# Performance work log

Measured on AMD Instinct MI355X. Metric: run time of the kernel, lower is better.

## Reference

```python
import jax, jax.numpy as jnp
import numpy as np

D_MODEL, D_STATE, D_CONV, EXPAND = 1024, 16, 4, 2
D_INNER = EXPAND * D_MODEL            # 2048
DT_RANK = -(-D_MODEL // 16)           # ceil(d_model/16) = 64
B_SZ, L_SEQ = 2, 2048


def setup_inputs() -> dict:
    key = jax.random.key(0)
    ks = jax.random.split(key, 8)
    s = 0.02
    x = jax.random.normal(ks[0], (B_SZ, L_SEQ, D_MODEL), dtype=jnp.float32)
    W_in = jax.random.normal(ks[1], (D_MODEL, 2 * D_INNER), dtype=jnp.float32) * s
    conv_w = jax.random.normal(ks[2], (D_INNER, 1, D_CONV), dtype=jnp.float32) * 0.1  # depthwise (O,I/g,K)
    conv_b = jnp.zeros((D_INNER,), dtype=jnp.float32)
    W_x = jax.random.normal(ks[3], (D_INNER, DT_RANK + 2 * D_STATE), dtype=jnp.float32) * s
    W_dt = jax.random.normal(ks[4], (DT_RANK, D_INNER), dtype=jnp.float32) * s
    b_dt = jax.random.normal(ks[5], (D_INNER,), dtype=jnp.float32) * 0.1
    A_log = jnp.log(jnp.tile(jnp.arange(1, D_STATE + 1, dtype=jnp.float32), (D_INNER, 1)))  # (d_in, n)
    D_param = jnp.ones((D_INNER,), dtype=jnp.float32)
    W_out = jax.random.normal(ks[6], (D_INNER, D_MODEL), dtype=jnp.float32) * s
    return {"x": x, "W_in": W_in, "conv_w": conv_w, "conv_b": conv_b,
            "W_x": W_x, "W_dt": W_dt, "b_dt": b_dt, "A_log": A_log,
            "D_param": D_param, "W_out": W_out}


def _mamba(x, W_in, conv_w, conv_b, W_x, W_dt, b_dt, A_log, D_param, W_out):
    b, l, _ = x.shape
    d_in, n = A_log.shape
    dt_rank = W_dt.shape[0]
    d_conv = conv_w.shape[-1]

    xr = x @ W_in                                  # (b, l, 2*d_in)
    xs, res = xr[..., :d_in], xr[..., d_in:]

    # causal depthwise conv1d (left pad d_conv-1, truncate to l)
    xc = jnp.transpose(xs, (0, 2, 1))              # (b, d_in, l)
    xc = jax.lax.conv_general_dilated(
        xc, conv_w, window_strides=(1,), padding=[(d_conv - 1, 0)],
        dimension_numbers=("NCH", "OIH", "NCH"), feature_group_count=d_in)
    xc = xc + conv_b[None, :, None]
    xc = jnp.transpose(xc, (0, 2, 1))              # (b, l, d_in)
    xc = jax.nn.silu(xc)

    # SSM parameterization
    x_dbl = xc @ W_x                               # (b, l, dt_rank + 2n)
    delta = jax.nn.softplus(x_dbl[..., :dt_rank] @ W_dt + b_dt)   # (b, l, d_in)
    Bm = x_dbl[..., dt_rank:dt_rank + n]           # (b, l, n)
    Cm = x_dbl[..., dt_rank + n:]                  # (b, l, n)
    A = -jnp.exp(A_log)                            # (d_in, n)

    deltaA = jnp.exp(jnp.einsum("bld,dn->bldn", delta, A))        # (b, l, d_in, n)
    dBu = jnp.einsum("bld,bld,bln->bldn", delta, xc, Bm)          # (b, l, d_in, n)

    def step(h, inp):
        dA_t, dBu_t, C_t = inp                     # (b,d,n), (b,d,n), (b,n)
        h = dA_t * h + dBu_t
        y_t = jnp.einsum("bdn,bn->bd", h, C_t)
        return h, y_t

    h0 = jnp.zeros((b, d_in, n), dtype=xc.dtype)
    _, ys = jax.lax.scan(
        step, h0,
        (jnp.transpose(deltaA, (1, 0, 2, 3)),
         jnp.transpose(dBu, (1, 0, 2, 3)),
         jnp.transpose(Cm, (1, 0, 2))))
    y = jnp.transpose(ys, (1, 0, 2)) + xc * D_param  # (b, l, d_in)

    y = y * jax.nn.silu(res)
    return y @ W_out                               # (b, l, d_model)


def reference(x, W_in, conv_w, conv_b, W_x, W_dt, b_dt, A_log, D_param, W_out):
    return _mamba(x, W_in, conv_w, conv_b, W_x, W_dt, b_dt, A_log, D_param, W_out)
```

## Files before the change

### kernel.cpp

```cpp
#include <hip/hip_runtime.h>
#include <math.h>

#define B_SZ    2
#define L_SEQ   2048
#define D_MODEL 1024
#define D_INNER 2048
#define D_STATE 16
#define DT_RANK 64
#define MM      (B_SZ * L_SEQ)
#define NCH     64
#define CLEN    (L_SEQ / NCH)
#define PFD     8

typedef _Float16 h8v __attribute__((ext_vector_type(8)));
typedef _Float16 h4v __attribute__((ext_vector_type(4)));
typedef float f32x4 __attribute__((ext_vector_type(4)));

__device__ __forceinline__ void gload16(const void* g, void* l) {
    __builtin_amdgcn_global_load_lds((const __attribute__((address_space(1))) void*)g,
                                     (__attribute__((address_space(3))) void*)l, 16, 0, 0);
}

__global__ __launch_bounds__(256) void prep(const float* __restrict__ x,
                                            _Float16* __restrict__ xf16,
                                            const float* __restrict__ W_in,
                                            _Float16* __restrict__ WinT,
                                            const float* __restrict__ W_x,
                                            _Float16* __restrict__ WxT,
                                            const float* __restrict__ W_dt,
                                            _Float16* __restrict__ WdtT,
                                            const float* __restrict__ W_out,
                                            _Float16* __restrict__ WoutT,
                                            const float* __restrict__ cw,
                                            float* __restrict__ cwT) {
    __shared__ float t[32][33];
    const int b = blockIdx.x;
    const float* W; _Float16* T; int K, N, tile;
    if (b < 4096)      { W = W_in;  T = WinT;  K = 1024; N = 4096; tile = b; }
    else if (b < 4288) { W = W_x;   T = WxT;   K = 2048; N = 96;   tile = b - 4096; }
    else if (b < 4416) { W = W_dt;  T = WdtT;  K = 64;   N = 2048; tile = b - 4288; }
    else if (b < 6464) { W = W_out; T = WoutT; K = 2048; N = 1024; tile = b - 4416; }
    else if (b < 10560) {
        int idx = (b - 6464) * 256 + threadIdx.x;
        float4 v = ((const float4*)x)[idx];
        h4v h = {(_Float16)v.x, (_Float16)v.y, (_Float16)v.z, (_Float16)v.w};
        *(h4v*)(xf16 + (size_t)idx * 4) = h;
        return;
    } else {
        for (int i = threadIdx.x; i < D_INNER * 4; i += 256) {
            int d = i >> 2, k = i & 3;
            cwT[k * D_INNER + d] = cw[i];
        }
        return;
    }
    const int ntx = N / 32;
    const int k0 = (tile / ntx) * 32, n0 = (tile % ntx) * 32;
    #pragma unroll
    for (int i = 0; i < 4; ++i) {
        int idx = threadIdx.x + i * 256;
        int r = idx >> 5, c = idx & 31;
        t[r][c] = W[(size_t)(k0 + r) * N + n0 + c];
    }
    __syncthreads();
    #pragma unroll
    for (int i = 0; i < 4; ++i) {
        int idx = threadIdx.x + i * 256;
        int n = idx >> 5, k = idx & 31;
        T[(size_t)(n0 + n) * K + k0 + k] = (_Float16)t[k][n];
    }
}

#define LDA_(mi, ks) (*(const h8v*)(smb + cb_ + rowA + (mi) * 2048 + ((ks) ? ps1 : ps0)))
#define LDB_(ni, ks) (*(const h8v*)(smb + cb_ + 32768 + rowB + (ni) * 2048 + ((ks) ? ps1 : ps0)))
#define PH(m0, m1) \
    _Pragma("unroll") \
    for (int ni = 0; ni < 4; ++ni) { \
        acc[m0][ni] = __builtin_amdgcn_mfma_f32_16x16x32_f16(aF0, bF[2 * ni],     acc[m0][ni], 0, 0, 0); \
        acc[m0][ni] = __builtin_amdgcn_mfma_f32_16x16x32_f16(aF1, bF[2 * ni + 1], acc[m0][ni], 0, 0, 0); \
        acc[m1][ni] = __builtin_amdgcn_mfma_f32_16x16x32_f16(aF2, bF[2 * ni],     acc[m1][ni], 0, 0, 0); \
        acc[m1][ni] = __builtin_amdgcn_mfma_f32_16x16x32_f16(aF3, bF[2 * ni + 1], acc[m1][ni], 0, 0, 0); \
    }

__global__ __launch_bounds__(512, 2) void gemm_k1(const _Float16* __restrict__ A,
                                                  const _Float16* __restrict__ Bt,
                                                  _Float16* __restrict__ H,
                                                  _Float16* __restrict__ Hg) {
    __shared__ _Float16 smem[65536];
    char* smb = (char*)smem;

    const int tid  = threadIdx.x;
    const int wave = tid >> 6, lane = tid & 63;
    const int wm = wave >> 2, wn = wave & 3;
    const int lm = lane & 15, lq = lane >> 4;
    const int bm = blockIdx.y * 256, bn = blockIdx.x * 256;

    const int ps0 = ((lq)     ^ (lm & 7)) << 4;
    const int ps1 = ((lq + 4) ^ (lm & 7)) << 4;
    const int rowA = (wm * 128 + lm) << 7;
    const int rowB = (wn * 64 + lm) << 7;

    const int srow  = lane >> 3;
    const int sslot = (lane & 7) ^ srow;
    const _Float16* pA = A  + (size_t)(bm + wave * 32 + srow) * 1024 + sslot * 8;
    const _Float16* pB = Bt + (size_t)(bn + wave * 32 + srow) * 1024 + sslot * 8;
    char* dA = smb + wave * 4096;
    char* dB = smb + 32768 + wave * 4096;

    f32x4 acc[8][4];
    #pragma unroll
    for (int i = 0; i < 8; ++i)
        #pragma unroll
        for (int j = 0; j < 4; ++j) acc[i][j] = (f32x4){0.f, 0.f, 0.f, 0.f};

    #pragma unroll
    for (int q = 0; q < 4; ++q) {
        gload16(pA + q * 8192, dA + q * 1024);
        gload16(pB + q * 8192, dB + q * 1024);
    }
    asm volatile("s_waitcnt vmcnt(0)" ::: "memory");
    __builtin_amdgcn_s_barrier();

    int cb_ = 0;
    for (int t = 0; t < 16; ++t) {
        const int nb_ = 65536 - cb_;
        const bool pf = (t < 15);
        const size_t kn = (size_t)(t + 1) * 64;

        h8v aF0, aF1, aF2, aF3;
        h8v bF[8];

        aF0 = LDA_(0, 0); aF1 = LDA_(0, 1); aF2 = LDA_(1, 0); aF3 = LDA_(1, 1);
        #pragma unroll
        for (int ni = 0; ni < 4; ++ni) { bF[2 * ni] = LDB_(ni, 0); bF[2 * ni + 1] = LDB_(ni, 1); }
        if (pf) {
            #pragma unroll
            for (int q = 0; q < 4; ++q) gload16(pA + kn + q * 8192, dA + nb_ + q * 1024);
        }
        __builtin_amdgcn_s_barrier();
        asm volatile("s_waitcnt lgkmcnt(0)" ::: "memory");
        __builtin_amdgcn_s_setprio(1);
        PH(0, 1);
        __builtin_amdgcn_s_setprio(0);
        __builtin_amdgcn_s_barrier();

        aF0 = LDA_(2, 0); aF1 = LDA_(2, 1); aF2 = LDA_(3, 0); aF3 = LDA_(3, 1);
        if (pf) {
            #pragma unroll
            for (int q = 0; q < 4; ++q) gload16(pB + kn + q * 8192, dB + nb_ + q * 1024);
        }
        __builtin_amdgcn_s_barrier();
        asm volatile("s_waitcnt lgkmcnt(0)" ::: "memory");
        __builtin_amdgcn_s_setprio(1);
        PH(2, 3);
        __builtin_amdgcn_s_setprio(0);
        __builtin_amdgcn_s_barrier();

        aF0 = LDA_(4, 0); aF1 = LDA_(4, 1); aF2 = LDA_(5, 0); aF3 = LDA_(5, 1);
        __builtin_amdgcn_s_barrier();
        asm volatile("s_waitcnt lgkmcnt(0)" ::: "memory");
        __builtin_amdgcn_s_setprio(1);
        PH(4, 5);
        __builtin_amdgcn_s_setprio(0);
        __builtin_amdgcn_s_barrier();

        aF0 = LDA_(6, 0); aF1 = LDA_(6, 1); aF2 = LDA_(7, 0); aF3 = LDA_(7, 1);
        asm volatile("s_waitcnt vmcnt(4)" ::: "memory");
        __builtin_amdgcn_s_barrier();
        asm volatile("s_waitcnt lgkmcnt(0)" ::: "memory");
        __builtin_amdgcn_s_setprio(1);
        PH(6, 7);
        __builtin_amdgcn_s_setprio(0);
        asm volatile("s_waitcnt vmcnt(0)" ::: "memory");
        __builtin_amdgcn_s_barrier();

        cb_ = nb_;
    }

    _Float16* ep = smem + wave * 2048;
    const bool gate = (bn >= 2048);
    _Float16* dst = gate ? Hg : H;
    const int cbase = bn + wn * 64 - (gate ? 2048 : 0);
    #pragma unroll
    for (int mi = 0; mi < 8; ++mi) {
        #pragma unroll
        for (int ni = 0; ni < 4; ++ni)
            #pragma unroll
            for (int r = 0; r < 4; ++r) {
                float v = acc[mi][ni][r];
                if (gate) v = v / (1.f + __expf(-v));
                ep[(lq * 4 + r) * 72 + ni * 16 + lm] = (_Float16)v;
            }
        int rowb = bm + wm * 128 + mi * 16;
        #pragma unroll
        for (int i = 0; i < 2; ++i) {
            int ch = lane + 64 * i;
            int row = ch >> 3, c8 = (ch & 7) * 8;
            *(h8v*)&dst[(size_t)(rowb + row) * 2048 + cbase + c8] =
                *(const h8v*)&ep[row * 72 + c8];
        }
    }
}
#undef LDA_
#undef LDB_
#undef PH

template<int EPI>
__global__ __launch_bounds__(256) void gemm_f16(const _Float16* __restrict__ A,
                                                const _Float16* __restrict__ Bt,
                                                const float* __restrict__ bias,
                                                float* __restrict__ C,
                                                _Float16* __restrict__ H,
                                                _Float16* __restrict__ Hg,
                                                int M, int N, int K, int ldc) {
    __shared__ _Float16 smemh[16384];

    const int tid = threadIdx.x;
    const int wave = tid >> 6, lane = tid & 63;
    const int bm = blockIdx.y * 128, bn = blockIdx.x * 128;

    const int lrow = lane >> 2, pc = lane & 3;
    const int ar = wave * 32 + lrow;
    const size_t gA = (size_t)(bm + ar) * K + ((pc ^ ((ar >> 1) & 3)) * 8);
    const size_t gB = (size_t)(bn + ar) * K + ((pc ^ ((ar >> 1) & 3)) * 8);
    const int lofs = (wave * 32) * 32;

    const int lm = lane & 15, lq = lane >> 4;
    const int rofs = (lq ^ ((lm >> 1) & 3)) * 8;
    const int wm = (wave >> 1) * 64, wn = (wave & 1) * 64;

    f32x4 acc[4][4];
    #pragma unroll
    for (int i = 0; i < 4; ++i)
        #pragma unroll
        for (int j = 0; j < 4; ++j) acc[i][j] = (f32x4){0.f, 0.f, 0.f, 0.f};

    gload16(A + gA, smemh + lofs);
    gload16(A + gA + (size_t)16 * K, smemh + lofs + 16 * 32);
    gload16(Bt + gB, smemh + 8192 + lofs);
    gload16(Bt + gB + (size_t)16 * K, smemh + 8192 + lofs + 16 * 32);
    __syncthreads();

    int kb = 0;
    for (int k0 = 0; k0 < K; k0 += 32, kb ^= 1) {
        if (k0 + 32 < K) {
            int nb = kb ^ 1;
            gload16(A + gA + k0 + 32, smemh + nb * 4096 + lofs);
            gload16(A + gA + k0 + 32 + (size_t)16 * K, smemh + nb * 4096 + lofs + 16 * 32);
            gload16(Bt + gB + k0 + 32, smemh + 8192 + nb * 4096 + lofs);
            gload16(Bt + gB + k0 + 32 + (size_t)16 * K, smemh + 8192 + nb * 4096 + lofs + 16 * 32);
        }

        const _Float16* sA = smemh + kb * 4096;
        const _Float16* sB = smemh + 8192 + kb * 4096;
        h8v fa[4], fb[4];
        #pragma unroll
        for (int i = 0; i < 4; ++i) {
            fa[i] = *(const h8v*)&sA[(wm + i * 16 + lm) * 32 + rofs];
            fb[i] = *(const h8v*)&sB[(wn + i * 16 + lm) * 32 + rofs];
        }
        #pragma unroll
        for (int mi = 0; mi < 4; ++mi)
            #pragma unroll
            for (int ni = 0; ni < 4; ++ni)
                acc[mi][ni] = __builtin_amdgcn_mfma_f32_16x16x32_f16(fa[mi], fb[ni], acc[mi][ni], 0, 0, 0);
        __syncthreads();
    }

    if (EPI == 0) {
        float* ep = (float*)smemh + wave * 1088;
        #pragma unroll
        for (int mi = 0; mi < 4; ++mi) {
            #pragma unroll
            for (int ni = 0; ni < 4; ++ni)
                #pragma unroll
                for (int r = 0; r < 4; ++r)
                    ep[(lq * 4 + r) * 68 + ni * 16 + lm] = acc[mi][ni][r];
            int rowb = bm + wm + mi * 16;
            #pragma unroll
            for (int i = 0; i < 4; ++i) {
                int ch = lane + 64 * i;
                int row = ch >> 4, c4 = (ch & 15) * 4;
                *(float4*)&C[(size_t)(rowb + row) * ldc + bn + wn + c4] =
                    *(const float4*)&ep[row * 68 + c4];
            }
        }
    } else {
        _Float16* ep = smemh + wave * 1152;
        const bool gate = (EPI == 2) && (bn >= 2048);
        _Float16* dst = gate ? Hg : H;
        const int cb = bn + wn - (gate ? 2048 : 0);
        #pragma unroll
        for (int mi = 0; mi < 4; ++mi) {
            #pragma unroll
            for (int ni = 0; ni < 4; ++ni) {
                int col = bn + wn + ni * 16 + lm;
                #pragma unroll
                for (int r = 0; r < 4; ++r) {
                    float v = acc[mi][ni][r];
                    if (EPI == 1) {
                        float a = v + bias[col];
                        v = (a > 20.f) ? a : log1pf(__expf(a));
                    } else if (gate) {
                        v = v / (1.f + __expf(-v));
                    }
                    ep[(lq * 4 + r) * 72 + ni * 16 + lm] = (_Float16)v;
                }
            }
            int rowb = bm + wm + mi * 16;
            #pragma unroll
            for (int i = 0; i < 2; ++i) {
                int ch = lane + 64 * i;
                int row = ch >> 3, c8 = (ch & 7) * 8;
                *(h8v*)&dst[(size_t)(rowb + row) * ldc + cb + c8] =
                    *(const h8v*)&ep[row * 72 + c8];
            }
        }
    }
}

__global__ __launch_bounds__(256) void gemm_xd(const _Float16* __restrict__ xch,
                                               const _Float16* __restrict__ WxT,
                                               _Float16* __restrict__ xdh,
                                               float* __restrict__ Bm,
                                               float* __restrict__ Cm) {
    __shared__ _Float16 sA[64 * 32];
    __shared__ _Float16 sB[96 * 32];
    const int tid = threadIdx.x;
    const int m0 = blockIdx.x * 64;
    const int wave = tid >> 6, lane = tid & 63;
    const int lm = lane & 15, lq = lane >> 4;
    const int rofs = (lq ^ ((lm >> 1) & 3)) * 8;

    const int wr = tid >> 2, wc = tid & 3, c0 = wc * 8;
    const int wofsA = wr * 32 + ((wc ^ ((wr >> 1) & 3)) * 8);
    const int wr2 = 64 + wr;
    const int wofsB2 = wr2 * 32 + ((wc ^ ((wr2 >> 1) & 3)) * 8);

    f32x4 acc[6];
    #pragma unroll
    for (int i = 0; i < 6; ++i) acc[i] = (f32x4){0.f, 0.f, 0.f, 0.f};

    h8v pA = *(const h8v*)(xch + (size_t)(m0 + wr) * D_INNER + c0);
    h8v pB0 = *(const h8v*)(WxT + (size_t)wr * D_INNER + c0);
    h8v pB1 = (tid < 128) ? *(const h8v*)(WxT + (size_t)wr2 * D_INNER + c0) : (h8v)0;

    for (int k0 = 0; k0 < D_INNER; k0 += 32) {
        *(h8v*)&sA[wofsA] = pA;
        *(h8v*)&sB[wofsA] = pB0;
        if (tid < 128) *(h8v*)&sB[wofsB2] = pB1;
        __syncthreads();

        if (k0 + 32 < D_INNER) {
            int kk = k0 + 32 + c0;
            pA = *(const h8v*)(xch + (size_t)(m0 + wr) * D_INNER + kk);
            pB0 = *(const h8v*)(WxT + (size_t)wr * D_INNER + kk);
            if (tid < 128) pB1 = *(const h8v*)(WxT + (size_t)wr2 * D_INNER + kk);
        }

        h8v fa = *(const h8v*)&sA[(wave * 16 + lm) * 32 + rofs];
        #pragma unroll
        for (int nf = 0; nf < 6; ++nf) {
            h8v fb = *(const h8v*)&sB[(nf * 16 + lm) * 32 + rofs];
            acc[nf] = __builtin_amdgcn_mfma_f32_16x16x32_f16(fa, fb, acc[nf], 0, 0, 0);
        }
        __syncthreads();
    }

    #pragma unroll
    for (int nf = 0; nf < 6; ++nf) {
        int col = nf * 16 + lm;
        #pragma unroll
        for (int r = 0; r < 4; ++r) {
            int row = m0 + wave * 16 + lq * 4 + r;
            float v = acc[nf][r];
            if (col < 64)      xdh[(size_t)row * 64 + col] = (_Float16)v;
            else if (col < 80) Bm[(size_t)row * 16 + (col - 64)] = v;
            else               Cm[(size_t)row * 16 + (col - 80)] = v;
        }
    }
}

__global__ __launch_bounds__(256) void conv_silu(const _Float16* __restrict__ xsh,
                                                 const float* __restrict__ cwT,
                                                 const float* __restrict__ cb,
                                                 _Float16* __restrict__ xch) {
    int idx = blockIdx.x * 256 + threadIdx.x;
    int d0 = (idx * 8) & (D_INNER - 1);
    int m  = (idx * 8) >> 11;
    int l  = m & (L_SEQ - 1);
    float acc[8];
    {
        float4 c0 = *(const float4*)&cb[d0];
        float4 c1 = *(const float4*)&cb[d0 + 4];
        acc[0] = c0.x; acc[1] = c0.y; acc[2] = c0.z; acc[3] = c0.w;
        acc[4] = c1.x; acc[5] = c1.y; acc[6] = c1.z; acc[7] = c1.w;
    }
    #pragma unroll
    for (int k = 0; k < 4; ++k) {
        int ll = l - 3 + k;
        if (ll >= 0) {
            h8v v = *(const h8v*)(xsh + (size_t)(m - 3 + k) * D_INNER + d0);
            float4 w0 = *(const float4*)&cwT[k * D_INNER + d0];
            float4 w1 = *(const float4*)&cwT[k * D_INNER + d0 + 4];
            acc[0] += (float)v[0] * w0.x; acc[1] += (float)v[1] * w0.y;
            acc[2] += (float)v[2] * w0.z; acc[3] += (float)v[3] * w0.w;
            acc[4] += (float)v[4] * w1.x; acc[5] += (float)v[5] * w1.y;
            acc[6] += (float)v[6] * w1.z; acc[7] += (float)v[7] * w1.w;
        }
    }
    h8v o;
    #pragma unroll
    for (int j = 0; j < 8; ++j) {
        float s = acc[j] / (1.f + __expf(-acc[j]));
        o[j] = (_Float16)s;
    }
    *(h8v*)(xch + (size_t)idx * 8) = o;
}

__global__ __launch_bounds__(256) void scan_part1(const _Float16* __restrict__ deltah,
                                                  const _Float16* __restrict__ xch,
                                                  const float* __restrict__ Bm,
                                                  const float* __restrict__ A_log,
                                                  float* __restrict__ hlocal,
                                                  float* __restrict__ Ssum) {
    const int t = threadIdx.x;
    const int d = blockIdx.x * 256 + t;
    const int c = blockIdx.y;
    const int b = blockIdx.z;

    float An[16];
    {
        const float4* ap = (const float4*)(A_log + (size_t)d * 16);
        #pragma unroll
        for (int q = 0; q < 4; ++q) {
            float4 v = ap[q];
            An[q * 4 + 0] = -__expf(v.x); An[q * 4 + 1] = -__expf(v.y);
            An[q * 4 + 2] = -__expf(v.z); An[q * 4 + 3] = -__expf(v.w);
        }
    }
    const float An0 = An[0];
    bool fast = An0 < 0.f;
    #pragma unroll
    for (int n = 0; n < 16; ++n)
        fast = fast && (fabsf(An[n] - (float)(n + 1) * An0) < 1e-3f * fabsf(An[n]));

    __shared__ float sB[CLEN][16];
    {
        size_t l0 = (size_t)(b * L_SEQ + c * CLEN) * 16;
        #pragma unroll
        for (int i = 0; i < (CLEN * 16) / 256; ++i) {
            int idx = t + i * 256;
            sB[idx >> 4][idx & 15] = Bm[l0 + idx];
        }
    }
    __syncthreads();

    float h[16];
    #pragma unroll
    for (int n = 0; n < 16; ++n) h[n] = 0.f;
    float S = 0.f;

    size_t base = (size_t)(b * L_SEQ + c * CLEN) * D_INNER + d;
    float bd[PFD], bx[PFD];
    #pragma unroll
    for (int i = 0; i < PFD; ++i) {
        bd[i] = (float)deltah[base + (size_t)i * D_INNER];
        bx[i] = (float)xch[base + (size_t)i * D_INNER];
    }

    if (fast) {
        for (int jb = 0; jb < CLEN; jb += PFD) {
            #pragma unroll
            for (int i = 0; i < PFD; ++i) {
                int j = jb + i;
                float dv = bd[i], xv = bx[i];
                int jn = j + PFD;
                if (jn < CLEN) {
                    bd[i] = (float)deltah[base + (size_t)jn * D_INNER];
                    bx[i] = (float)xch[base + (size_t)jn * D_INNER];
                }
                S += dv;
                float dbx = dv * xv;
                float r = __expf(dv * An0);
                float pw = r;
                #pragma unroll
                for (int n = 0; n < 16; ++n) {
                    h[n] = pw * h[n] + dbx * sB[j][n];
                    pw *= r;
                }
            }
        }
    } else {
        for (int jb = 0; jb < CLEN; jb += PFD) {
            #pragma unroll
            for (int i = 0; i < PFD; ++i) {
                int j = jb + i;
                float dv = bd[i], xv = bx[i];
                int jn = j + PFD;
                if (jn < CLEN) {
                    bd[i] = (float)deltah[base + (size_t)jn * D_INNER];
                    bx[i] = (float)xch[base + (size_t)jn * D_INNER];
                }
                S += dv;
                float dbx = dv * xv;
                #pragma unroll
                for (int n = 0; n < 16; ++n)
                    h[n] = __expf(dv * An[n]) * h[n] + dbx * sB[j][n];
            }
        }
    }

    size_t o = ((size_t)(b * NCH + c) * D_INNER + d) * 16;
    float4* hp = (float4*)(hlocal + o);
    #pragma unroll
    for (int q = 0; q < 4; ++q)
        hp[q] = make_float4(h[q * 4], h[q * 4 + 1], h[q * 4 + 2], h[q * 4 + 3]);
    Ssum[(size_t)(b * NCH + c) * D_INNER + d] = S;
}

__global__ __launch_bounds__(256) void scan_combine(const float* __restrict__ hlocal,
                                                    const float* __restrict__ Ssum,
                                                    const float* __restrict__ A_log,
                                                    float* __restrict__ h0buf) {
    int gid = blockIdx.x * 256 + threadIdx.x;
    int n = gid & 15;
    int d = (gid >> 4) & (D_INNER - 1);
    int b = gid >> 15;
    float An = -__expf(A_log[(size_t)d * 16 + n]);
    float H = 0.f;
    float pS[4], pH[4];
    #pragma unroll
    for (int i = 0; i < 4; ++i) {
        size_t sc = (size_t)(b * NCH + i) * D_INNER + d;
        pS[i] = Ssum[sc];
        pH[i] = hlocal[sc * 16 + n];
    }
    for (int cb = 0; cb < NCH; cb += 4) {
        #pragma unroll
        for (int i = 0; i < 4; ++i) {
            int c = cb + i;
            float S = pS[i], hl = pH[i];
            int cn = c + 4;
            if (cn < NCH) {
                size_t sc = (size_t)(b * NCH + cn) * D_INNER + d;
                pS[i] = Ssum[sc];
                pH[i] = hlocal[sc * 16 + n];
            }
            size_t o = ((size_t)(b * NCH + c) * D_INNER + d) * 16 + n;
            h0buf[o] = H;
            H = __expf(An * S) * H + hl;
        }
    }
}

__global__ __launch_bounds__(256) void scan_part2(const _Float16* __restrict__ deltah,
                                                  const _Float16* __restrict__ xch,
                                                  const float* __restrict__ Bm,
                                                  const float* __restrict__ Cm,
                                                  const float* __restrict__ h0buf,
                                                  const float* __restrict__ A_log,
                                                  const float* __restrict__ Dp,
                                                  const _Float16* __restrict__ sresh,
                                                  _Float16* __restrict__ yhalf) {
    const int t = threadIdx.x;
    const int d = blockIdx.x * 256 + t;
    const int c = blockIdx.y;
    const int b = blockIdx.z;

    float An[16];
    {
        const float4* ap = (const float4*)(A_log + (size_t)d * 16);
        #pragma unroll
        for (int q = 0; q < 4; ++q) {
            float4 v = ap[q];
            An[q * 4 + 0] = -__expf(v.x); An[q * 4 + 1] = -__expf(v.y);
            An[q * 4 + 2] = -__expf(v.z); An[q * 4 + 3] = -__expf(v.w);
        }
    }
    const float An0 = An[0];
    bool fast = An0 < 0.f;
    #pragma unroll
    for (int n = 0; n < 16; ++n)
        fast = fast && (fabsf(An[n] - (float)(n + 1) * An0) < 1e-3f * fabsf(An[n]));

    __shared__ float sB[CLEN][16];
    __shared__ float sC[CLEN][16];
    {
        size_t l0 = (size_t)(b * L_SEQ + c * CLEN) * 16;
        #pragma unroll
        for (int i = 0; i < (CLEN * 16) / 256; ++i) {
            int idx = t + i * 256;
            sB[idx >> 4][idx & 15] = Bm[l0 + idx];
            sC[idx >> 4][idx & 15] = Cm[l0 + idx];
        }
    }
    __syncthreads();

    float h[16];
    {
        size_t o = ((size_t)(b * NCH + c) * D_INNER + d) * 16;
        const float4* hp = (const float4*)(h0buf + o);
        #pragma unroll
        for (int q = 0; q < 4; ++q) {
            float4 v = hp[q];
            h[q * 4 + 0] = v.x; h[q * 4 + 1] = v.y;
            h[q * 4 + 2] = v.z; h[q * 4 + 3] = v.w;
        }
    }
    const float Dv = Dp[d];

    size_t base = (size_t)(b * L_SEQ + c * CLEN) * D_INNER + d;
    float bd[PFD], bx[PFD], bg[PFD];
    #pragma unroll
    for (int i = 0; i < PFD; ++i) {
        bd[i] = (float)deltah[base + (size_t)i * D_INNER];
        bx[i] = (float)xch[base + (size_t)i * D_INNER];
        bg[i] = (float)sresh[base + (size_t)i * D_INNER];
    }

    if (fast) {
        for (int jb = 0; jb < CLEN; jb += PFD) {
            #pragma unroll
            for (int i = 0; i < PFD; ++i) {
                int j = jb + i;
                float dv = bd[i], xv = bx[i], gv = bg[i];
                int jn = j + PFD;
                if (jn < CLEN) {
                    bd[i] = (float)deltah[base + (size_t)jn * D_INNER];
                    bx[i] = (float)xch[base + (size_t)jn * D_INNER];
                    bg[i] = (float)sresh[base + (size_t)jn * D_INNER];
                }
                float dbx = dv * xv;
                float r = __expf(dv * An0);
                float pw = r;
                float y = 0.f;
                #pragma unroll
                for (int n = 0; n < 16; ++n) {
                    h[n] = pw * h[n] + dbx * sB[j][n];
                    y += h[n] * sC[j][n];
                    pw *= r;
                }
                float yv = (y + xv * Dv) * gv;
                yhalf[base + (size_t)j * D_INNER] = (_Float16)yv;
            }
        }
    } else {
        for (int jb = 0; jb < CLEN; jb += PFD) {
            #pragma unroll
            for (int i = 0; i < PFD; ++i) {
                int j = jb + i;
                float dv = bd[i], xv = bx[i], gv = bg[i];
                int jn = j + PFD;
                if (jn < CLEN) {
                    bd[i] = (float)deltah[base + (size_t)jn * D_INNER];
                    bx[i] = (float)xch[base + (size_t)jn * D_INNER];
                    bg[i] = (float)sresh[base + (size_t)jn * D_INNER];
                }
                float dbx = dv * xv;
                float y = 0.f;
                #pragma unroll
                for (int n = 0; n < 16; ++n) {
                    h[n] = __expf(dv * An[n]) * h[n] + dbx * sB[j][n];
                    y += h[n] * sC[j][n];
                }
                float yv = (y + xv * Dv) * gv;
                yhalf[base + (size_t)j * D_INNER] = (_Float16)yv;
            }
        }
    }
}

extern "C" void kernel_launch(void* const* d_in, const int* in_sizes, int n_in,
                              void* d_out, int out_size, void* d_ws, size_t ws_size,
                              hipStream_t stream) {
    const float* x      = (const float*)d_in[0];
    const float* W_in   = (const float*)d_in[1];
    const float* conv_w = (const float*)d_in[2];
    const float* conv_b = (const float*)d_in[3];
    const float* W_x    = (const float*)d_in[4];
    const float* W_dt   = (const float*)d_in[5];
    const float* b_dt   = (const float*)d_in[6];
    const float* A_log  = (const float*)d_in[7];
    const float* D_par  = (const float*)d_in[8];
    const float* W_out  = (const float*)d_in[9];
    float* out = (float*)d_out;

    char* wsb = (char*)d_ws;
    _Float16*  xsh    = (_Float16*)(wsb + 0);
    _Float16*  sresh  = (_Float16*)(wsb + 16777216);
    _Float16*  deltah = (_Float16*)(wsb + 33554432);
    _Float16*  xch    = (_Float16*)(wsb + 50331648);
    _Float16*  xf16   = (_Float16*)(wsb + 67108864);
    _Float16*  WinT   = (_Float16*)(wsb + 75497472);
    _Float16*  yhalf  = (_Float16*)(wsb + 67108864);
    _Float16*  WxT    = (_Float16*)(wsb + 83886080);
    _Float16*  WdtT   = (_Float16*)(wsb + 84279296);
    _Float16*  xdh    = (_Float16*)(wsb + 84541440);
    float*     Bbuf   = (float*)(wsb + 85065728);
    float*     Cbuf   = (float*)(wsb + 85327872);
    float*     Ssum   = (float*)(wsb + 85590016);
    float*     hloc   = (float*)(wsb + 86638592);
    float*     h0buf  = (float*)(wsb + 103415808);
    _Float16*  WoutT  = (_Float16*)(wsb + 120193024);
    float*     cwT    = (float*)(wsb + 124387328);

    dim3 blk(256);

    prep<<<dim3(10561), blk, 0, stream>>>(x, xf16, W_in, WinT, W_x, WxT,
                                          W_dt, WdtT, W_out, WoutT, conv_w, cwT);
    gemm_k1<<<dim3(16, 16), dim3(512), 0, stream>>>(xf16, WinT, xsh, sresh);
    conv_silu<<<dim3((size_t)MM * D_INNER / 8 / 256), blk, 0, stream>>>(xsh, cwT, conv_b, xch);
    gemm_xd<<<dim3(MM / 64), blk, 0, stream>>>(xch, WxT, xdh, Bbuf, Cbuf);
    gemm_f16<1><<<dim3(16, 32), blk, 0, stream>>>(
        xdh, WdtT, b_dt, nullptr, deltah, nullptr, MM, D_INNER, DT_RANK, D_INNER);
    scan_part1<<<dim3(D_INNER / 256, NCH, B_SZ), blk, 0, stream>>>(deltah, xch, Bbuf, A_log, hloc, Ssum);
    scan_combine<<<dim3(B_SZ * D_INNER * 16 / 256), blk, 0, stream>>>(hloc, Ssum, A_log, h0buf);
    scan_part2<<<dim3(D_INNER / 256, NCH, B_SZ), blk, 0, stream>>>(deltah, xch, Bbuf, Cbuf, h0buf, A_log, D_par, sresh, yhalf);
    gemm_f16<0><<<dim3(8, 32), blk, 0, stream>>>(
        yhalf, WoutT, nullptr, out, nullptr, nullptr, MM, D_MODEL, D_INNER, D_MODEL);
}
```

Before: 316.4 us.

## Restructure in-projection GEMM main loop: k-split phases, XCD-aware block remap, sched barriers

```diff
diff --git a/kernel.cpp b/kernel.cpp
--- a/kernel.cpp
+++ b/kernel.cpp
@@ -70,16 +70,21 @@
     }
 }
 
-#define LDA_(mi, ks) (*(const h8v*)(smb + cb_ + rowA + (mi) * 2048 + ((ks) ? ps1 : ps0)))
-#define LDB_(ni, ks) (*(const h8v*)(smb + cb_ + 32768 + rowB + (ni) * 2048 + ((ks) ? ps1 : ps0)))
-#define PH(m0, m1) \
-    _Pragma("unroll") \
-    for (int ni = 0; ni < 4; ++ni) { \
-        acc[m0][ni] = __builtin_amdgcn_mfma_f32_16x16x32_f16(aF0, bF[2 * ni],     acc[m0][ni], 0, 0, 0); \
-        acc[m0][ni] = __builtin_amdgcn_mfma_f32_16x16x32_f16(aF1, bF[2 * ni + 1], acc[m0][ni], 0, 0, 0); \
-        acc[m1][ni] = __builtin_amdgcn_mfma_f32_16x16x32_f16(aF2, bF[2 * ni],     acc[m1][ni], 0, 0, 0); \
-        acc[m1][ni] = __builtin_amdgcn_mfma_f32_16x16x32_f16(aF3, bF[2 * ni + 1], acc[m1][ni], 0, 0, 0); \
-    }
+#define MF(d, a, b) d = __builtin_amdgcn_mfma_f32_16x16x32_f16(a, b, d, 0, 0, 0)
+#define MF16(mb)                                                              \
+    MF(acc[(mb)+0][0], aF0, bF0); MF(acc[(mb)+0][1], aF0, bF1);               \
+    MF(acc[(mb)+0][2], aF0, bF2); MF(acc[(mb)+0][3], aF0, bF3);               \
+    MF(acc[(mb)+1][0], aF1, bF0); MF(acc[(mb)+1][1], aF1, bF1);               \
+    MF(acc[(mb)+1][2], aF1, bF2); MF(acc[(mb)+1][3], aF1, bF3);               \
+    MF(acc[(mb)+2][0], aF2, bF0); MF(acc[(mb)+2][1], aF2, bF1);               \
+    MF(acc[(mb)+2][2], aF2, bF2); MF(acc[(mb)+2][3], aF2, bF3);               \
+    MF(acc[(mb)+3][0], aF3, bF0); MF(acc[(mb)+3][1], aF3, bF1);               \
+    MF(acc[(mb)+3][2], aF3, bF2); MF(acc[(mb)+3][3], aF3, bF3);
+#define PRE_MFMA                                                              \
+    __builtin_amdgcn_s_barrier();                                             \
+    asm volatile("s_waitcnt lgkmcnt(0)" ::: "memory");                        \
+    __builtin_amdgcn_sched_barrier(0);                                        \
+    __builtin_amdgcn_s_setprio(1);
 
 __global__ __launch_bounds__(512, 2) void gemm_k1(const _Float16* __restrict__ A,
                                                   const _Float16* __restrict__ Bt,
@@ -92,19 +97,24 @@
     const int wave = tid >> 6, lane = tid & 63;
     const int wm = wave >> 2, wn = wave & 3;
     const int lm = lane & 15, lq = lane >> 4;
-    const int bm = blockIdx.y * 256, bn = blockIdx.x * 256;
-
-    const int ps0 = ((lq)     ^ (lm & 7)) << 4;
-    const int ps1 = ((lq + 4) ^ (lm & 7)) << 4;
-    const int rowA = (wm * 128 + lm) << 7;
-    const int rowB = (wn * 64 + lm) << 7;
-
-    const int srow  = lane >> 3;
-    const int sslot = (lane & 7) ^ srow;
-    const _Float16* pA = A  + (size_t)(bm + wave * 32 + srow) * 1024 + sslot * 8;
-    const _Float16* pB = Bt + (size_t)(bn + wave * 32 + srow) * 1024 + sslot * 8;
-    char* dA = smb + wave * 4096;
-    char* dB = smb + 32768 + wave * 4096;
+
+    const int bid = blockIdx.y * 16 + blockIdx.x;
+    const int xcd = bid & 7, idx = bid >> 3;
+    const int bx = ((xcd & 1) << 3) + (idx & 7);
+    const int by = ((xcd >> 1) << 2) + (idx >> 3);
+    const int bm = by * 256, bn = bx * 256;
+
+    const int sw  = lm & 7;
+    const int PS0 = ((lq)     ^ sw) << 4;
+    const int PS1 = ((lq + 4) ^ sw) << 4;
+    const int rA0 = (wm * 128 + lm) << 7;
+    const int rB0 = 32768 + ((wn * 64 + lm) << 7);
+
+    const int srow   = tid >> 3;
+    const int sslot8 = ((tid & 7) ^ ((tid >> 3) & 7)) * 8;
+    const _Float16* pAs = A  + (size_t)(bm + srow) * 1024 + sslot8;
+    const _Float16* pBs = Bt + (size_t)(bn + srow) * 1024 + sslot8;
+    const int wq16 = wave * 1024;
 
     f32x4 acc[8][4];
     #pragma unroll
@@ -113,67 +123,77 @@
         for (int j = 0; j < 4; ++j) acc[i][j] = (f32x4){0.f, 0.f, 0.f, 0.f};
 
     #pragma unroll
-    for (int q = 0; q < 4; ++q) {
-        gload16(pA + q * 8192, dA + q * 1024);
-        gload16(pB + q * 8192, dB + q * 1024);
+    for (int j = 0; j < 4; ++j) {
+        gload16(pAs + j * 65536, smb + j * 8192 + wq16);
+        gload16(pBs + j * 65536, smb + 32768 + j * 8192 + wq16);
     }
     asm volatile("s_waitcnt vmcnt(0)" ::: "memory");
     __builtin_amdgcn_s_barrier();
 
-    int cb_ = 0;
     for (int t = 0; t < 16; ++t) {
-        const int nb_ = 65536 - cb_;
+        const char* buf = smb + ((t & 1) << 16);
+        char* nsl = smb + (((t + 1) & 1) << 16);
         const bool pf = (t < 15);
         const size_t kn = (size_t)(t + 1) * 64;
 
-        h8v aF0, aF1, aF2, aF3;
-        h8v bF[8];
-
-        aF0 = LDA_(0, 0); aF1 = LDA_(0, 1); aF2 = LDA_(1, 0); aF3 = LDA_(1, 1);
-        #pragma unroll
-        for (int ni = 0; ni < 4; ++ni) { bF[2 * ni] = LDB_(ni, 0); bF[2 * ni + 1] = LDB_(ni, 1); }
+        h8v aF0, aF1, aF2, aF3, bF0, bF1, bF2, bF3;
+
+        aF0 = *(const h8v*)(buf + rA0 +    0 + PS0);
+        aF1 = *(const h8v*)(buf + rA0 + 2048 + PS0);
+        aF2 = *(const h8v*)(buf + rA0 + 4096 + PS0);
+        aF3 = *(const h8v*)(buf + rA0 + 6144 + PS0);
+        bF0 = *(const h8v*)(buf + rB0 +    0 + PS0);
+        bF1 = *(const h8v*)(buf + rB0 + 2048 + PS0);
+        bF2 = *(const h8v*)(buf + rB0 + 4096 + PS0);
+        bF3 = *(const h8v*)(buf + rB0 + 6144 + PS0);
         if (pf) {
-            #pragma unroll
-            for (int q = 0; q < 4; ++q) gload16(pA + kn + q * 8192, dA + nb_ + q * 1024);
-        }
-        __builtin_amdgcn_s_barrier();
-        asm volatile("s_waitcnt lgkmcnt(0)" ::: "memory");
-        __builtin_amdgcn_s_setprio(1);
-        PH(0, 1);
+            gload16(pAs + kn,          nsl +         wq16);
+            gload16(pAs + kn +  65536, nsl +  8192 + wq16);
+            gload16(pAs + kn + 131072, nsl + 16384 + wq16);
+            gload16(pAs + kn + 196608, nsl + 24576 + wq16);
+        }
+        PRE_MFMA
+        MF16(0)
         __builtin_amdgcn_s_setprio(0);
         __builtin_amdgcn_s_barrier();
 
-        aF0 = LDA_(2, 0); aF1 = LDA_(2, 1); aF2 = LDA_(3, 0); aF3 = LDA_(3, 1);
+        aF0 = *(const h8v*)(buf + rA0 +  8192 + PS0);
+        aF1 = *(const h8v*)(buf + rA0 + 10240 + PS0);
+        aF2 = *(const h8v*)(buf + rA0 + 12288 + PS0);
+        aF3 = *(const h8v*)(buf + rA0 + 14336 + PS0);
         if (pf) {
-            #pragma unroll
-            for (int q = 0; q < 4; ++q) gload16(pB + kn + q * 8192, dB + nb_ + q * 1024);
-        }
-        __builtin_amdgcn_s_barrier();
-        asm volatile("s_waitcnt lgkmcnt(0)" ::: "memory");
-        __builtin_amdgcn_s_setprio(1);
-        PH(2, 3);
+            gload16(pBs + kn,          nsl + 32768 + wq16);
+            gload16(pBs + kn +  65536, nsl + 40960 + wq16);
+            gload16(pBs + kn + 131072, nsl + 49152 + wq16);
+            gload16(pBs + kn + 196608, nsl + 57344 + wq16);
+        }
+        PRE_MFMA
+        MF16(4)
         __builtin_amdgcn_s_setprio(0);
         __builtin_amdgcn_s_barrier();
 
-        aF0 = LDA_(4, 0); aF1 = LDA_(4, 1); aF2 = LDA_(5, 0); aF3 = LDA_(5, 1);
-        __builtin_amdgcn_s_barrier();
-        asm volatile("s_waitcnt lgkmcnt(0)" ::: "memory");
-        __builtin_amdgcn_s_setprio(1);
-        PH(4, 5);
+        aF0 = *(const h8v*)(buf + rA0 +    0 + PS1);
+        aF1 = *(const h8v*)(buf + rA0 + 2048 + PS1);
+        aF2 = *(const h8v*)(buf + rA0 + 4096 + PS1);
+        aF3 = *(const h8v*)(buf + rA0 + 6144 + PS1);
+        bF0 = *(const h8v*)(buf + rB0 +    0 + PS1);
+        bF1 = *(const h8v*)(buf + rB0 + 2048 + PS1);
+        bF2 = *(const h8v*)(buf + rB0 + 4096 + PS1);
+        bF3 = *(const h8v*)(buf + rB0 + 6144 + PS1);
+        PRE_MFMA
+        MF16(0)
         __builtin_amdgcn_s_setprio(0);
         __builtin_amdgcn_s_barrier();
 
-        aF0 = LDA_(6, 0); aF1 = LDA_(6, 1); aF2 = LDA_(7, 0); aF3 = LDA_(7, 1);
-        asm volatile("s_waitcnt vmcnt(4)" ::: "memory");
-        __builtin_amdgcn_s_barrier();
-        asm volatile("s_waitcnt lgkmcnt(0)" ::: "memory");
-        __builtin_amdgcn_s_setprio(1);
-        PH(6, 7);
+        aF0 = *(const h8v*)(buf + rA0 +  8192 + PS1);
+        aF1 = *(const h8v*)(buf + rA0 + 10240 + PS1);
+        aF2 = *(const h8v*)(buf + rA0 + 12288 + PS1);
+        aF3 = *(const h8v*)(buf + rA0 + 14336 + PS1);
+        PRE_MFMA
+        MF16(4)
         __builtin_amdgcn_s_setprio(0);
         asm volatile("s_waitcnt vmcnt(0)" ::: "memory");
         __builtin_amdgcn_s_barrier();
-
-        cb_ = nb_;
     }
 
     _Float16* ep = smem + wave * 2048;
@@ -200,9 +220,9 @@
         }
     }
 }
-#undef LDA_
-#undef LDB_
-#undef PH
+#undef MF
+#undef MF16
+#undef PRE_MFMA
 
 template<int EPI>
 __global__ __launch_bounds__(256) void gemm_f16(const _Float16* __restrict__ A,
```

Measured after the change: 480.1 us. +51.7%, slower.
